# Kernel optimization log

Hardware: AMD Instinct MI355X
Metric: run time of the kernel (lower is better)

Reference implementation:

```python
import jax, jax.numpy as jnp
import numpy as np
from jax import lax

H = 106      # hidden size
IN = 100     # input feature size
S = 512      # sequence length (time-major)
B = 256      # batch
N_REST = 10  # layers 2..6 of lstm1 (5) + all 5 layers of lstm2, all 106->106


def _lstm_layer(x, Wih, Whh, bih, bhh):
    """Single LSTM layer, PyTorch gate order (i, f, g, o). x: (S, B, in)."""
    # Precompute input contribution for all timesteps at once: (S, B, 4H)
    gx = jnp.einsum('sbi,gi->sbg', x, Wih) + bih + bhh

    def step(carry, g_t):
        h, c = carry
        g = g_t + h @ Whh.T                      # (B, 4H)
        i, f, gg, o = jnp.split(g, 4, axis=-1)
        i = jax.nn.sigmoid(i)
        f = jax.nn.sigmoid(f)
        gg = jnp.tanh(gg)
        o = jax.nn.sigmoid(o)
        c = f * c + i * gg
        h = o * jnp.tanh(c)
        return (h, c), h

    b = x.shape[1]
    h0 = jnp.zeros((b, H), x.dtype)
    c0 = jnp.zeros((b, H), x.dtype)
    _, ys = lax.scan(step, (h0, c0), gx)
    return ys  # (S, B, H)


def setup_inputs() -> dict:
    key = jax.random.key(0)
    ks = jax.random.split(key, 10)
    k = 1.0 / np.sqrt(H)  # PyTorch LSTM default uniform init bound
    u = lambda kk, shape: jax.random.uniform(kk, shape, jnp.float32, -k, k)

    noise = jax.random.normal(ks[0], (S, B, IN), jnp.float32)
    # First layer: input dim 100
    W_ih0 = u(ks[1], (4 * H, IN))
    W_hh0 = u(ks[2], (4 * H, H))
    b_ih0 = u(ks[3], (4 * H,))
    b_hh0 = u(ks[4], (4 * H,))
    # Remaining 10 layers: input dim 106, stacked
    W_ih = u(ks[5], (N_REST, 4 * H, H))
    W_hh = u(ks[6], (N_REST, 4 * H, H))
    b_ih = u(ks[7], (N_REST, 4 * H))
    b_hh = u(ks[8], (N_REST, 4 * H))
    return {"noise": noise, "W_ih0": W_ih0, "W_hh0": W_hh0, "b_ih0": b_ih0,
            "b_hh0": b_hh0, "W_ih": W_ih, "W_hh": W_hh, "b_ih": b_ih, "b_hh": b_hh}


def reference(noise, W_ih0, W_hh0, b_ih0, b_hh0, W_ih, W_hh, b_ih, b_hh):
    x = _lstm_layer(noise, W_ih0, W_hh0, b_ih0, b_hh0)

    def layer_step(xc, params):
        Wih, Whh, bih, bhh = params
        return _lstm_layer(xc, Wih, Whh, bih, bhh), None

    x, _ = lax.scan(layer_step, x, (W_ih, W_hh, b_ih, b_hh))
    return x  # (S, B, H)
```

## Files before the change

kernel.cpp:

```cpp
#include <hip/hip_runtime.h>
#include <cmath>


namespace {
constexpr int H = 106, G4 = 424, SEQ = 512, BB = 256, KIN0 = 100;
constexpr int UST = 264;
constexpr int GST = 436;
constexpr int NTHR = 896;
constexpr int RGN = 16;
constexpr int NLAYER = 11;
constexpr int RD = 8;
constexpr int REL = 56;
constexpr size_t CNT_STRIDE = 16;
constexpr size_t RING_OFF_B = 65536;
constexpr size_t RING_PER_L = (size_t)RD * BB * REL;

using f16x8 = __attribute__((ext_vector_type(8))) _Float16;
using f32x4 = __attribute__((ext_vector_type(4))) float;
typedef unsigned long long u64;

__device__ __forceinline__ u64 ald(const u64* p) {
    return __hip_atomic_load(p, __ATOMIC_RELAXED, __HIP_MEMORY_SCOPE_AGENT);
}
__device__ __forceinline__ void ast(u64* p, u64 v) {
    __hip_atomic_store(p, v, __ATOMIC_RELAXED, __HIP_MEMORY_SCOPE_AGENT);
}
__device__ __forceinline__ void spinc(const unsigned* p, unsigned tgt) {
    while (__hip_atomic_load(p, __ATOMIC_RELAXED, __HIP_MEMORY_SCOPE_AGENT) < tgt)
        __builtin_amdgcn_s_sleep(8);
}
__device__ __forceinline__ float fast_tanh(float x) {
    float t = __expf(2.0f * x);
    return 1.0f - 2.0f / (t + 1.0f);
}
__device__ __forceinline__ float act_gate(float g, bool istanh) {
    float s = istanh ? 2.0f * g : g;
    float r = 1.0f / (1.0f + __expf(-s));
    return istanh ? 2.0f * r - 1.0f : r;
}
__device__ __forceinline__ unsigned packh2(float a, float b) {
    unsigned lo = (unsigned)__builtin_bit_cast(unsigned short, (_Float16)a);
    unsigned hi = (unsigned)__builtin_bit_cast(unsigned short, (_Float16)b);
    return (hi << 16) | lo;
}

__global__ __launch_bounds__(NTHR)
__attribute__((amdgpu_waves_per_eu(4, 4)))
void lstm_wave(const float* __restrict__ noise,
               float* __restrict__ yout,
               unsigned* cnt, u64* ring,
               const float* __restrict__ W_ih0, const float* __restrict__ W_hh0,
               const float* __restrict__ b_ih0, const float* __restrict__ b_hh0,
               const float* __restrict__ W_ih,  const float* __restrict__ W_hh,
               const float* __restrict__ b_ih,  const float* __restrict__ b_hh)
{
    const int l = blockIdx.x / RGN;
    const int rg = blockIdx.x % RGN;
    const bool LAST = (l == NLAYER - 1);
    const int K_IN = (l == 0) ? KIN0 : H;

    const float* Wih = (l == 0) ? W_ih0 : W_ih + (size_t)(l - 1) * G4 * H;
    const float* Whh = (l == 0) ? W_hh0 : W_hh + (size_t)(l - 1) * G4 * H;
    const float* pbi = (l == 0) ? b_ih0 : b_ih + (size_t)(l - 1) * G4;
    const float* pbh = (l == 0) ? b_hh0 : b_hh + (size_t)(l - 1) * G4;

    unsigned* cons_my = cnt + (size_t)(l * RGN + rg) * CNT_STRIDE;
    unsigned* cons_in = cnt + (size_t)((l - 1) * RGN + rg) * CNT_STRIDE;
    u64* ring_in  = ring + (size_t)(l - 1) * RING_PER_L;
    u64* ring_out = ring + (size_t)l * RING_PER_L;

    __shared__ __align__(16) _Float16 su[16 * UST];
    __shared__ float gl[16 * GST];

    const int tid = threadIdx.x;
    const int w = tid >> 6, lane = tid & 63;
    const int l16 = lane & 15, kg = lane >> 4;
    const int lm = tid / 56, ld = tid % 56;

    f16x8 bf[2][8];
    float bias[2];
    #pragma unroll
    for (int t = 0; t < 2; ++t) {
        const int n = 16 * (2 * w + t) + l16;
        const bool valid = n < G4;
        const float* pwx = Wih + (size_t)(valid ? n : 0) * K_IN;
        const float* pwh = Whh + (size_t)(valid ? n : 0) * H;
        #pragma unroll
        for (int q = 0; q < 8; ++q) {
            f16x8 v;
            #pragma unroll
            for (int e = 0; e < 8; ++e) {
                const int k = 32 * q + 8 * kg + e;
                float f = 0.0f;
                if (valid) {
                    if (k < 128) { if (k < K_IN) f = pwx[k]; }
                    else { const int kh = k - 128; if (kh < H) f = pwh[kh]; }
                }
                v[e] = (_Float16)f;
            }
            bf[t][q] = v;
        }
        bias[t] = valid ? (pbi[n] + pbh[n]) : 0.0f;
    }

    for (int i = tid; i < 16 * (UST / 2); i += NTHR) ((unsigned*)su)[i] = 0;
    float c0 = 0.0f, c1 = 0.0f;
    __syncthreads();
    {
        unsigned xr = 0;
        if (l == 0) {
            if (ld < 50) {
                const float2 v = *(const float2*)(noise + ((size_t)rg * 16 + lm) * KIN0 + 2 * ld);
                xr = packh2(v.x, v.y);
            }
        } else {
            const u64* p = ring_in + ((size_t)0 * BB + rg * 16 + lm) * REL + ld;
            u64 v = ald(p);
            while ((unsigned)(v >> 32) != 1u) { __builtin_amdgcn_s_sleep(1); v = ald(p); }
            xr = (unsigned)v;
        }
        ((unsigned*)su)[lm * 132 + ld] = xr;
    }
    __syncthreads();

    const _Float16* abase = su + (size_t)l16 * UST + 8 * kg;
    const int um = tid / 53, up = tid % 53;

    for (int s = 0; s < SEQ; ++s) {
        u64 v = 0; unsigned xr = 0;
        const bool wantx = (s + 1 < SEQ);
        const u64* pin = ring_in + ((size_t)((s + 1) % RD) * BB + rg * 16 + lm) * REL + ld;
        if (wantx) {
            if (l == 0) {
                if (ld < 50) {
                    const float2 t = *(const float2*)(noise + ((size_t)(s + 1) * BB + rg * 16 + lm) * KIN0 + 2 * ld);
                    xr = packh2(t.x, t.y);
                }
            } else {
                v = ald(pin);
            }
        }
        if (tid == 0 && !LAST && s >= RD) spinc(cons_my, (unsigned)(s - RD + 2));

        f32x4 acc[2] = {{0, 0, 0, 0}, {0, 0, 0, 0}};
        #pragma unroll
        for (int q = 0; q < 4; ++q) {
            const f16x8 a = *(const f16x8*)(abase + 32 * q);
            acc[0] = __builtin_amdgcn_mfma_f32_16x16x32_f16(a, bf[0][q], acc[0], 0, 0, 0);
            acc[1] = __builtin_amdgcn_mfma_f32_16x16x32_f16(a, bf[1][q], acc[1], 0, 0, 0);
        }
        __syncthreads();

        #pragma unroll
        for (int q = 4; q < 8; ++q) {
            const f16x8 a = *(const f16x8*)(abase + 32 * q);
            acc[0] = __builtin_amdgcn_mfma_f32_16x16x32_f16(a, bf[0][q], acc[0], 0, 0, 0);
            acc[1] = __builtin_amdgcn_mfma_f32_16x16x32_f16(a, bf[1][q], acc[1], 0, 0, 0);
        }
        #pragma unroll
        for (int t = 0; t < 2; ++t) {
            const int n = 16 * (2 * w + t) + l16;
            if (n < G4) {
                const bool istanh = (n >= 2 * H) && (n < 3 * H);
                #pragma unroll
                for (int r = 0; r < 4; ++r)
                    gl[(4 * kg + r) * GST + n] = act_gate(acc[t][r] + bias[t], istanh);
            }
        }
        if (wantx) {
            if (l > 0) {
                const unsigned expt = (unsigned)(s + 2);
                while ((unsigned)(v >> 32) != expt) { __builtin_amdgcn_s_sleep(1); v = ald(pin); }
                xr = (unsigned)v;
            }
            ((unsigned*)su)[lm * 132 + ld] = xr;
        }
        __syncthreads();

        if (tid < 848) {
            const float* gm = gl + um * GST;
            const float i0 = gm[2 * up],         i1 = gm[2 * up + 1];
            const float f0 = gm[H + 2 * up],     f1 = gm[H + 2 * up + 1];
            const float g0 = gm[2 * H + 2 * up], g1 = gm[2 * H + 2 * up + 1];
            const float o0 = gm[3 * H + 2 * up], o1 = gm[3 * H + 2 * up + 1];
            c0 = fmaf(f0, c0, i0 * g0);
            c1 = fmaf(f1, c1, i1 * g1);
            const float h0 = o0 * fast_tanh(c0);
            const float h1 = o1 * fast_tanh(c1);
            const unsigned hw = packh2(h0, h1);
            ((unsigned*)su)[um * 132 + 64 + up] = hw;
            if (LAST) {
                *(float2*)(yout + ((size_t)s * BB + rg * 16 + um) * H + 2 * up) =
                    make_float2(h0, h1);
            } else {
                ast(ring_out + ((size_t)(s % RD) * BB + rg * 16 + um) * REL + up,
                    ((u64)(unsigned)(s + 1) << 32) | hw);
            }
        } else if (!LAST) {
            const int t2 = tid - 848, m = t2 / 3, dd = t2 % 3;
            ast(ring_out + ((size_t)(s % RD) * BB + rg * 16 + m) * REL + 53 + dd,
                (u64)(unsigned)(s + 1) << 32);
        }
        __syncthreads();

        if (tid == 0 && l > 0 && s + 1 < SEQ)
            __hip_atomic_store(cons_in, (unsigned)(s + 2),
                               __ATOMIC_RELAXED, __HIP_MEMORY_SCOPE_AGENT);
    }
}
}

extern "C" void kernel_launch(void* const* d_in, const int* in_sizes, int n_in,
                              void* d_out, int out_size, void* d_ws, size_t ws_size,
                              hipStream_t stream) {
    const float* noise = (const float*)d_in[0];
    const float* W_ih0 = (const float*)d_in[1];
    const float* W_hh0 = (const float*)d_in[2];
    const float* b_ih0 = (const float*)d_in[3];
    const float* b_hh0 = (const float*)d_in[4];
    const float* W_ih  = (const float*)d_in[5];
    const float* W_hh  = (const float*)d_in[6];
    const float* b_ih  = (const float*)d_in[7];
    const float* b_hh  = (const float*)d_in[8];

    const size_t clear_bytes = RING_OFF_B + (size_t)NLAYER * RING_PER_L * sizeof(u64);
    hipMemsetAsync(d_ws, 0, clear_bytes, stream);

    unsigned* cnt = (unsigned*)d_ws;
    u64* ring = (u64*)((char*)d_ws + RING_OFF_B);

    lstm_wave<<<dim3(NLAYER * RGN), dim3(NTHR), 0, stream>>>(
        noise, (float*)d_out, cnt, ring,
        W_ih0, W_hh0, b_ih0, b_hh0, W_ih, W_hh, b_ih, b_hh);
}
```

Measured before the change: 1.476 ms.

## Double-buffer x input in LDS, drop mid-step barrier, batch ring backpressure

Adds a second slot for the incoming layer input in the shared A-operand row, alternated by timestep parity, so the next x can be written without waiting for all waves to finish reading the current one. This removes one __syncthreads per timestep. The ring depth doubles so the producer only checks consumer progress every 8 steps instead of every step. The gate reads are also vectorised to float2, and LDS use per row grows to make room for the extra slot.

Measured after the change: 1.419 ms. 1.04x faster.

```diff
diff --git a/kernel.cpp b/kernel.cpp
--- a/kernel.cpp
+++ b/kernel.cpp
@@ -4,12 +4,12 @@
 
 namespace {
 constexpr int H = 106, G4 = 424, SEQ = 512, BB = 256, KIN0 = 100;
-constexpr int UST = 264;
+constexpr int UST = 392;
 constexpr int GST = 436;
 constexpr int NTHR = 896;
 constexpr int RGN = 16;
 constexpr int NLAYER = 11;
-constexpr int RD = 8;
+constexpr int RD = 16;
 constexpr int REL = 56;
 constexpr size_t CNT_STRIDE = 16;
 constexpr size_t RING_OFF_B = 65536;
@@ -119,11 +119,10 @@
             while ((unsigned)(v >> 32) != 1u) { __builtin_amdgcn_s_sleep(1); v = ald(p); }
             xr = (unsigned)v;
         }
-        ((unsigned*)su)[lm * 132 + ld] = xr;
+        ((unsigned*)su)[lm * 196 + ld] = xr;
     }
     __syncthreads();
 
-    const _Float16* abase = su + (size_t)l16 * UST + 8 * kg;
     const int um = tid / 53, up = tid % 53;
 
     for (int s = 0; s < SEQ; ++s) {
@@ -140,20 +139,22 @@
                 v = ald(pin);
             }
         }
-        if (tid == 0 && !LAST && s >= RD) spinc(cons_my, (unsigned)(s - RD + 2));
-
+        if (tid == 0 && !LAST && s >= RD && (s & 7) == 0)
+            spinc(cons_my, (unsigned)(s - 8));
+
+        const _Float16* arow = su + (size_t)l16 * UST;
+        const _Float16* ax = arow + (s & 1) * 128 + 8 * kg;
         f32x4 acc[2] = {{0, 0, 0, 0}, {0, 0, 0, 0}};
         #pragma unroll
         for (int q = 0; q < 4; ++q) {
-            const f16x8 a = *(const f16x8*)(abase + 32 * q);
+            const f16x8 a = *(const f16x8*)(ax + 32 * q);
             acc[0] = __builtin_amdgcn_mfma_f32_16x16x32_f16(a, bf[0][q], acc[0], 0, 0, 0);
             acc[1] = __builtin_amdgcn_mfma_f32_16x16x32_f16(a, bf[1][q], acc[1], 0, 0, 0);
         }
-        __syncthreads();
-
+        const _Float16* ah = arow + 256 + 8 * kg;
         #pragma unroll
         for (int q = 4; q < 8; ++q) {
-            const f16x8 a = *(const f16x8*)(abase + 32 * q);
+            const f16x8 a = *(const f16x8*)(ah + 32 * (q - 4));
             acc[0] = __builtin_amdgcn_mfma_f32_16x16x32_f16(a, bf[0][q], acc[0], 0, 0, 0);
             acc[1] = __builtin_amdgcn_mfma_f32_16x16x32_f16(a, bf[1][q], acc[1], 0, 0, 0);
         }
@@ -173,22 +174,22 @@
                 while ((unsigned)(v >> 32) != expt) { __builtin_amdgcn_s_sleep(1); v = ald(pin); }
                 xr = (unsigned)v;
             }
-            ((unsigned*)su)[lm * 132 + ld] = xr;
+            ((unsigned*)su)[lm * 196 + ((s + 1) & 1) * 64 + ld] = xr;
         }
         __syncthreads();
 
         if (tid < 848) {
             const float* gm = gl + um * GST;
-            const float i0 = gm[2 * up],         i1 = gm[2 * up + 1];
-            const float f0 = gm[H + 2 * up],     f1 = gm[H + 2 * up + 1];
-            const float g0 = gm[2 * H + 2 * up], g1 = gm[2 * H + 2 * up + 1];
-            const float o0 = gm[3 * H + 2 * up], o1 = gm[3 * H + 2 * up + 1];
-            c0 = fmaf(f0, c0, i0 * g0);
-            c1 = fmaf(f1, c1, i1 * g1);
-            const float h0 = o0 * fast_tanh(c0);
-            const float h1 = o1 * fast_tanh(c1);
+            const float2 vi = *(const float2*)(gm + 2 * up);
+            const float2 vf = *(const float2*)(gm + H + 2 * up);
+            const float2 vg = *(const float2*)(gm + 2 * H + 2 * up);
+            const float2 vo = *(const float2*)(gm + 3 * H + 2 * up);
+            c0 = fmaf(vf.x, c0, vi.x * vg.x);
+            c1 = fmaf(vf.y, c1, vi.y * vg.y);
+            const float h0 = vo.x * fast_tanh(c0);
+            const float h1 = vo.y * fast_tanh(c1);
             const unsigned hw = packh2(h0, h1);
-            ((unsigned*)su)[um * 132 + 64 + up] = hw;
+            ((unsigned*)su)[um * 196 + 128 + up] = hw;
             if (LAST) {
                 *(float2*)(yout + ((size_t)s * BB + rg * 16 + um) * H + 2 * up) =
                     make_float2(h0, h1);
```
